# Optimization experiments

Measured on AMD Instinct MI355X. Metric: run time of the kernel, lower is better.

Reference implementation:

```python
import jax, jax.numpy as jnp
import numpy as np

N, E, F_IN, HID, HEADS, NG, NC = 50000, 800000, 128, 64, 4, 64, 10
NEG_SLOPE = 0.2


def gat_conv(h_in, src, dst, W, att_src, att_dst, bias, heads, out_ch, concat, num_nodes):
    # h_in: [N, Fin]; W: [Fin, heads*out_ch]; att_*: [heads, out_ch]; bias: [heads*out_ch] or [out_ch]
    h = (h_in @ W).reshape(num_nodes, heads, out_ch)            # [N,H,C]
    a_src = jnp.sum(h * att_src, axis=-1)                        # [N,H]
    a_dst = jnp.sum(h * att_dst, axis=-1)                        # [N,H]
    alpha = jax.nn.leaky_relu(a_src[src] + a_dst[dst], NEG_SLOPE)  # [Etot,H]
    # softmax over incoming edges per destination node
    amax = jax.ops.segment_max(alpha, dst, num_segments=num_nodes)
    amax = jnp.where(jnp.isfinite(amax), amax, 0.0)
    ex = jnp.exp(alpha - amax[dst])
    denom = jax.ops.segment_sum(ex, dst, num_segments=num_nodes)
    w = ex / (denom[dst] + 1e-16)                                # [Etot,H]
    msg = h[src] * w[:, :, None]                                 # [Etot,H,C]
    out = jax.ops.segment_sum(msg, dst, num_segments=num_nodes)  # [N,H,C]
    out = out.reshape(num_nodes, heads * out_ch) if concat else out.mean(axis=1)
    return out + bias


def setup_inputs() -> dict:
    key = jax.random.key(0)
    ks = jax.random.split(key, 20)
    s = lambda k, shp, f: (jax.random.normal(k, shp, jnp.float32) * f)
    return {
        "x": jax.random.normal(ks[0], (N, F_IN), jnp.float32),
        "edge_index": jax.random.randint(ks[1], (2, E), 0, N, jnp.int32),
        "batch": jax.random.randint(ks[2], (N,), 0, NG, jnp.int32),
        "W_proj": s(ks[3], (F_IN, HID), 0.05), "b_proj": jnp.zeros((HID,), jnp.float32),
        "W1": s(ks[4], (HID, HEADS * HID), 0.05),
        "att_src1": s(ks[5], (HEADS, HID), 0.1), "att_dst1": s(ks[6], (HEADS, HID), 0.1),
        "b1": jnp.zeros((HEADS * HID,), jnp.float32),
        "W2": s(ks[7], (HEADS * HID, HID), 0.05),
        "att_src2": s(ks[8], (1, HID), 0.1), "att_dst2": s(ks[9], (1, HID), 0.1),
        "b2": jnp.zeros((HID,), jnp.float32),
        "W_fc1": s(ks[10], (HID, HID // 2), 0.05), "b_fc1": jnp.zeros((HID // 2,), jnp.float32),
        "W_fc2": s(ks[11], (HID // 2, NC), 0.05), "b_fc2": jnp.zeros((NC,), jnp.float32),
    }


def reference(x, edge_index, batch, W_proj, b_proj, W1, att_src1, att_dst1, b1,
              W2, att_src2, att_dst2, b2, W_fc1, b_fc1, W_fc2, b_fc2):
    n = x.shape[0]
    loops = jnp.arange(n, dtype=edge_index.dtype)  # PyG GATConv add_self_loops=True
    src = jnp.concatenate([edge_index[0], loops])
    dst = jnp.concatenate([edge_index[1], loops])
    h = jax.nn.relu(x @ W_proj + b_proj)                                  # feature_proj + relu
    h = gat_conv(h, src, dst, W1, att_src1, att_dst1, b1, HEADS, HID, True, n)
    h = jax.nn.leaky_relu(h, NEG_SLOPE)                                    # dropout = identity (eval)
    h = gat_conv(h, src, dst, W2, att_src2, att_dst2, b2, 1, HID, False, n)
    h = jax.nn.leaky_relu(h, NEG_SLOPE)
    cnt = jax.ops.segment_sum(jnp.ones((n,), h.dtype), batch, num_segments=NG)
    gmean = jax.ops.segment_sum(h, batch, num_segments=NG) / jnp.maximum(cnt, 1.0)[:, None]
    gmax = jax.ops.segment_max(h, batch, num_segments=NG)
    gmax = jnp.where(jnp.isfinite(gmax), gmax, 0.0)
    g = gmean + gmax
    g = jax.nn.relu(g @ W_fc1 + b_fc1)
    return jax.nn.log_softmax(g @ W_fc2 + b_fc2, axis=1)
```

## Files before the change

### kernel.cpp

```cpp
#include <hip/hip_runtime.h>
#include <math.h>

#define NN 50000
#define EE 800000
#define ET 850000
#define FIN 128
#define HD 64
#define NH 4
#define NGR 64
#define NCL 10
#define NEG 0.2f

typedef unsigned short u16;
typedef unsigned char u8;
typedef unsigned int u32;
typedef __attribute__((ext_vector_type(8))) short short8;
typedef __attribute__((ext_vector_type(4))) float f32x4;

__device__ __forceinline__ float lrelu(float x){ return x > 0.f ? x : NEG * x; }

__device__ __forceinline__ float wsum(float v){
#pragma unroll
  for (int o = 32; o > 0; o >>= 1) v += __shfl_xor(v, o, 64);
  return v;
}
__device__ __forceinline__ float wmax(float v){
#pragma unroll
  for (int o = 32; o > 0; o >>= 1) v = fmaxf(v, __shfl_xor(v, o, 64));
  return v;
}
__device__ __forceinline__ int esrc(const int* ei, int e){ return e < EE ? ei[e] : e - EE; }
__device__ __forceinline__ int edst(const int* ei, int e){ return e < EE ? ei[EE + e] : e - EE; }

__device__ __forceinline__ unsigned f2key(float f){
  unsigned u = __float_as_uint(f);
  return (u & 0x80000000u) ? ~u : (u | 0x80000000u);
}
__device__ __forceinline__ float key2f(unsigned k){
  return (k & 0x80000000u) ? __uint_as_float(k & 0x7fffffffu) : __uint_as_float(~k);
}

__device__ __forceinline__ u16 f2b(float f){
  u32 u = __float_as_uint(f);
  u32 r = (u + 0x7FFFu + ((u >> 16) & 1u)) >> 16;
  return (u16)r;
}
__device__ __forceinline__ float b2f(u16 b){ return __uint_as_float(((u32)b) << 16); }
__device__ __forceinline__ u32 pkbf16(float lo, float hi){
  u32 r;
  asm("v_cvt_pk_bf16_f32 %0, %1, %2" : "=v"(r) : "v"(lo), "v"(hi));
  return r;
}
__device__ __forceinline__ u8 f2fp8(float f){
  return (u8)__builtin_amdgcn_cvt_pk_fp8_f32(f, 0.f, 0, false);
}
__device__ __forceinline__ int rl(int v, int idx){ return __builtin_amdgcn_readlane(v, idx); }
__device__ __forceinline__ float rlf(float v, int idx){
  return __uint_as_float((u32)__builtin_amdgcn_readlane((int)__float_as_uint(v), idx));
}

template<int K, int NOUT, int CPW, bool RELU_BIAS, bool DOTS1, bool DOTS2, bool AF32, bool F8OUT>
__device__ __forceinline__ void gemm_body(int bid, u16* As, float* sred,
            const void* __restrict__ Av, const float* __restrict__ Bf,
            const float* __restrict__ bias, const float* __restrict__ att_s, const float* __restrict__ att_d,
            void* __restrict__ Cv, float* __restrict__ a_s, float* __restrict__ a_d){
  const u16* A = (const u16*)Av;
  const float* Af = (const float*)Av;
  constexpr int KT = K/32;
  constexpr int NT = CPW/16;
  constexpr int LDK = K + 8;
  int t = threadIdx.x, w = t >> 6, l = t & 63;
  int c0 = w*CPW;
  int l16 = l & 15, kg = l >> 4;

  short8 bf[KT*NT];
#pragma unroll
  for (int kt = 0; kt < KT; ++kt)
#pragma unroll
    for (int nt = 0; nt < NT; ++nt){
      int kbase = kt*32 + kg*8;
      int col = c0 + nt*16 + l16;
      short8 v;
#pragma unroll
      for (int j = 0; j < 8; ++j) v[j] = (short)f2b(Bf[(size_t)(kbase + j)*NOUT + col]);
      bf[kt*NT + nt] = v;
    }
  float bv = 0.f;
  if (RELU_BIAS) bv = bias[c0 + l16];
  float asv[NT], adv[NT];
  if (DOTS1 || DOTS2){
#pragma unroll
    for (int nt = 0; nt < NT; ++nt){
      asv[nt] = att_s[c0 + nt*16 + l16];
      adv[nt] = att_d[c0 + nt*16 + l16];
    }
  }

  for (int ch = 0; ch < 2; ++ch){
    int nb = (bid*2 + ch)*64;
    if (nb >= NN) break;
    __syncthreads();
    constexpr int UPR = K/8;
    for (int u = t; u < 64*UPR; u += 256){
      int r = u / UPR, c = u % UPR;
      int n = nb + r;
      uint4 v = make_uint4(0u,0u,0u,0u);
      if (AF32){
        if (n < NN){
          float4 f0 = *(const float4*)&Af[(size_t)n*K + c*8];
          float4 f1 = *(const float4*)&Af[(size_t)n*K + c*8 + 4];
          v = make_uint4(pkbf16(f0.x,f0.y), pkbf16(f0.z,f0.w), pkbf16(f1.x,f1.y), pkbf16(f1.z,f1.w));
        }
      } else {
        if (n < NN) v = *(const uint4*)&A[(size_t)n*K + c*8];
      }
      *(uint4*)&As[r*LDK + c*8] = v;
    }
    __syncthreads();
#pragma unroll
    for (int rt = 0; rt < 4; ++rt){
      short8 af[KT];
#pragma unroll
      for (int kt = 0; kt < KT; ++kt)
        af[kt] = *(const short8*)&As[(rt*16 + l16)*LDK + kt*32 + kg*8];
      f32x4 acc[NT];
#pragma unroll
      for (int nt = 0; nt < NT; ++nt){
        acc[nt] = (f32x4){0.f,0.f,0.f,0.f};
#pragma unroll
        for (int kt = 0; kt < KT; ++kt)
          acc[nt] = __builtin_amdgcn_mfma_f32_16x16x32_bf16(af[kt], bf[kt*NT + nt], acc[nt], 0, 0, 0);
      }
      int rbase = nb + rt*16 + kg*4;
#pragma unroll
      for (int nt = 0; nt < NT; ++nt)
#pragma unroll
        for (int r4 = 0; r4 < 4; ++r4){
          int n = rbase + r4;
          if (n < NN){
            float v = acc[nt][r4];
            if (RELU_BIAS) v = fmaxf(v + bv, 0.f);
            if (F8OUT) ((u8*)Cv)[(size_t)n*NOUT + c0 + nt*16 + l16] = f2fp8(v);
            else       ((u16*)Cv)[(size_t)n*NOUT + c0 + nt*16 + l16] = f2b(v);
          }
        }
      if (DOTS1){
#pragma unroll
        for (int r4 = 0; r4 < 4; ++r4){
          float ps = 0.f, pd = 0.f;
#pragma unroll
          for (int nt = 0; nt < NT; ++nt){
            ps = fmaf(acc[nt][r4], asv[nt], ps);
            pd = fmaf(acc[nt][r4], adv[nt], pd);
          }
#pragma unroll
          for (int o = 1; o < 16; o <<= 1){
            ps += __shfl_xor(ps, o, 64);
            pd += __shfl_xor(pd, o, 64);
          }
          int n = rbase + r4;
          if (l16 == 0 && n < NN){ a_s[n*NH + w] = ps; a_d[n*NH + w] = pd; }
        }
      }
      if (DOTS2){
#pragma unroll
        for (int r4 = 0; r4 < 4; ++r4){
          float ps = acc[0][r4]*asv[0];
          float pd = acc[0][r4]*adv[0];
#pragma unroll
          for (int o = 1; o < 16; o <<= 1){
            ps += __shfl_xor(ps, o, 64);
            pd += __shfl_xor(pd, o, 64);
          }
          if (l16 == 0){
            int row = rt*16 + kg*4 + r4;
            sred[(w*64 + row)*2]     = ps;
            sred[(w*64 + row)*2 + 1] = pd;
          }
        }
      }
    }
    if (DOTS2){
      __syncthreads();
      if (t < 64){
        int n = nb + t;
        if (n < NN){
          float s = sred[t*2] + sred[(64+t)*2] + sred[(128+t)*2] + sred[(192+t)*2];
          float d = sred[t*2+1] + sred[(64+t)*2+1] + sred[(128+t)*2+1] + sred[(192+t)*2+1];
          a_s[n] = s; a_d[n] = d;
        }
      }
    }
  }
}

__global__ __launch_bounds__(256) void k_hist_proj(const int* __restrict__ ei, int* __restrict__ cnt,
            int* __restrict__ rank,
            const float* __restrict__ x, const float* __restrict__ Wp, const float* __restrict__ bp,
            u16* __restrict__ h0b, int gb){
  __shared__ u16 As[64*(FIN+8)];
  int b = blockIdx.x;
  if (b < gb){
    gemm_body<128, 64, 16, true, false, false, true, false>(b, As, nullptr, x, Wp, bp, nullptr, nullptr, h0b, nullptr, nullptr);
  } else {
    int base = (b - gb)*1024;
#pragma unroll
    for (int k = 0; k < 4; ++k){
      int e = base + k*256 + threadIdx.x;
      if (e < ET){
        int d = edst(ei, e);
        rank[e] = atomicAdd(&cnt[d], 1);
      }
    }
  }
}

__global__ void k_bsum(const int* __restrict__ cnt, int* __restrict__ bsums){
  int b = blockIdx.x, t = threadIdx.x;
  int i = b*256 + t;
  int v = (i < NN) ? cnt[i] : 0;
  float s = wsum((float)v);
  __shared__ float ws4[4];
  if ((t & 63) == 0) ws4[t >> 6] = s;
  __syncthreads();
  if (t == 0) bsums[b] = (int)(ws4[0] + ws4[1] + ws4[2] + ws4[3] + 0.5f);
}

__global__ void k_boff(const int* __restrict__ bsums, int* __restrict__ boffs, int nb){
  __shared__ int s[256];
  int t = threadIdx.x;
  int v = (t < nb) ? bsums[t] : 0;
  s[t] = v; __syncthreads();
  for (int d = 1; d < 256; d <<= 1){
    int xv = (t >= d) ? s[t-d] : 0;
    __syncthreads();
    s[t] += xv;
    __syncthreads();
  }
  if (t < nb) boffs[t] = s[t] - v;
}

__global__ void k_off(const int* __restrict__ cnt, const int* __restrict__ boffs,
                      int* __restrict__ off){
  int b = blockIdx.x, t = threadIdx.x;
  int i = b*256 + t;
  __shared__ int s[256];
  int v = (i < NN) ? cnt[i] : 0;
  s[t] = v; __syncthreads();
  for (int d = 1; d < 256; d <<= 1){
    int xv = (t >= d) ? s[t-d] : 0;
    __syncthreads();
    s[t] += xv;
    __syncthreads();
  }
  int excl = s[t] - v;
  if (i < NN) off[i] = boffs[b] + excl;
  if (i == NN - 1) off[NN] = boffs[b] + s[t];
}

__global__ __launch_bounds__(256) void k_scat_feat1(const int* __restrict__ ei, const int* __restrict__ off,
            const int* __restrict__ rank, u16* __restrict__ csrc,
            const u16* __restrict__ h0b, const float* __restrict__ W1,
            const float* __restrict__ as1, const float* __restrict__ ad1,
            u8* __restrict__ h1f8, float* __restrict__ a_s, float* __restrict__ a_d, int gb){
  __shared__ u16 As[64*(HD+8)];
  int b = blockIdx.x;
  if (b < gb){
    gemm_body<64, 256, 64, false, true, false, false, true>(b, As, nullptr, h0b, W1, nullptr, as1, ad1, h1f8, a_s, a_d);
  } else {
    int base = (b - gb)*1024;
#pragma unroll
    for (int k = 0; k < 4; ++k){
      int e = base + k*256 + threadIdx.x;
      if (e < ET){
        int d = edst(ei, e);
        int s = esrc(ei, e);
        csrc[off[d] + rank[e]] = (u16)s;
      }
    }
  }
}

__global__ __launch_bounds__(256) void k_feat2(const u16* __restrict__ h1outb, const float* __restrict__ W2,
            const float* __restrict__ as2, const float* __restrict__ ad2,
            u16* __restrict__ h2b, float* __restrict__ a_s, float* __restrict__ a_d){
  __shared__ u16 As[64*(256+8)];
  __shared__ float sred[4*64*2];
  gemm_body<256, 64, 16, false, false, true, false, false>(blockIdx.x, As, sred, h1outb, W2, nullptr, as2, ad2, h2b, a_s, a_d);
}

__global__ __launch_bounds__(256) void k_gat1(const u8* __restrict__ h1f8, const float* __restrict__ a_s,
                       const float* __restrict__ a_d, const int* __restrict__ off,
                       const u16* __restrict__ csrc, const float* __restrict__ b1,
                       u16* __restrict__ h1outb){
  __shared__ float lw[4][4][68];
  int wv = threadIdx.x >> 6, l = threadIdx.x & 63;
  int n = blockIdx.x*4 + wv;
  if (n >= NN) return;
  int e0 = off[n], e1 = off[n+1], deg = e1 - e0;
  int j16 = l & 15, h = l >> 4;
  float adst = a_d[n*NH + h];
  float acc0 = 0.f, acc1 = 0.f, acc2 = 0.f, acc3 = 0.f;
  const u8* base = h1f8 + 4*l;

#define GAT1_FMA8(wrd, wq) { \
  acc0 = fmaf(__builtin_amdgcn_cvt_f32_fp8((int)(wrd), 0), wq, acc0); \
  acc1 = fmaf(__builtin_amdgcn_cvt_f32_fp8((int)(wrd), 1), wq, acc1); \
  acc2 = fmaf(__builtin_amdgcn_cvt_f32_fp8((int)(wrd), 2), wq, acc2); \
  acc3 = fmaf(__builtin_amdgcn_cvt_f32_fp8((int)(wrd), 3), wq, acc3); }

  if (deg <= 64){
    int sreg[4]; float wreg[4];
#pragma unroll
    for (int c = 0; c < 4; ++c){
      int idx = c*16 + j16;
      int s = (idx < deg) ? (int)csrc[e0 + idx] : 0;
      sreg[c] = s;
      wreg[c] = (idx < deg) ? lrelu(a_s[s*NH + h] + adst) : -3.0e38f;
    }
    float m = fmaxf(fmaxf(wreg[0], wreg[1]), fmaxf(wreg[2], wreg[3]));
#pragma unroll
    for (int o2 = 1; o2 < 16; o2 <<= 1) m = fmaxf(m, __shfl_xor(m, o2, 64));
    float se = 0.f;
#pragma unroll
    for (int c = 0; c < 4; ++c){
      int idx = c*16 + j16;
      float wc = (idx < deg) ? __expf(wreg[c] - m) : 0.f;
      wreg[c] = wc; se += wc;
    }
#pragma unroll
    for (int o2 = 1; o2 < 16; o2 <<= 1) se += __shfl_xor(se, o2, 64);
    float inv = 1.f / (se + 1e-16f);
#pragma unroll
    for (int c = 0; c < 4; ++c) lw[wv][h][c*16 + j16] = wreg[c] * inv;

#pragma unroll
    for (int c = 0; c < 4; ++c){
      int cbase = c*16;
      if (cbase < deg){
        int cnt = deg - cbase; if (cnt > 16) cnt = 16;
        int j2 = 0;
        for (; j2 + 8 <= cnt; j2 += 8){
          float4 wqa = *(const float4*)&lw[wv][h][cbase + j2];
          float4 wqb = *(const float4*)&lw[wv][h][cbase + j2 + 4];
          int s0 = rl(sreg[c], j2),   s1 = rl(sreg[c], j2+1);
          int s2 = rl(sreg[c], j2+2), s3 = rl(sreg[c], j2+3);
          int s4 = rl(sreg[c], j2+4), s5 = rl(sreg[c], j2+5);
          int s6 = rl(sreg[c], j2+6), s7 = rl(sreg[c], j2+7);
          u32 w0 = *(const u32*)(base + (size_t)(u32)s0*256);
          u32 w1 = *(const u32*)(base + (size_t)(u32)s1*256);
          u32 w2 = *(const u32*)(base + (size_t)(u32)s2*256);
          u32 w3 = *(const u32*)(base + (size_t)(u32)s3*256);
          u32 w4 = *(const u32*)(base + (size_t)(u32)s4*256);
          u32 w5 = *(const u32*)(base + (size_t)(u32)s5*256);
          u32 w6 = *(const u32*)(base + (size_t)(u32)s6*256);
          u32 w7 = *(const u32*)(base + (size_t)(u32)s7*256);
          GAT1_FMA8(w0, wqa.x) GAT1_FMA8(w1, wqa.y) GAT1_FMA8(w2, wqa.z) GAT1_FMA8(w3, wqa.w)
          GAT1_FMA8(w4, wqb.x) GAT1_FMA8(w5, wqb.y) GAT1_FMA8(w6, wqb.z) GAT1_FMA8(w7, wqb.w)
        }
        for (; j2 + 4 <= cnt; j2 += 4){
          float4 wq = *(const float4*)&lw[wv][h][cbase + j2];
          int s0 = rl(sreg[c], j2),   s1 = rl(sreg[c], j2+1);
          int s2 = rl(sreg[c], j2+2), s3 = rl(sreg[c], j2+3);
          u32 w0 = *(const u32*)(base + (size_t)(u32)s0*256);
          u32 w1 = *(const u32*)(base + (size_t)(u32)s1*256);
          u32 w2 = *(const u32*)(base + (size_t)(u32)s2*256);
          u32 w3 = *(const u32*)(base + (size_t)(u32)s3*256);
          GAT1_FMA8(w0, wq.x) GAT1_FMA8(w1, wq.y) GAT1_FMA8(w2, wq.z) GAT1_FMA8(w3, wq.w)
        }
        for (; j2 < cnt; ++j2){
          float wqs = lw[wv][h][cbase + j2];
          int s = rl(sreg[c], j2);
          u32 wd = *(const u32*)(base + (size_t)(u32)s*256);
          GAT1_FMA8(wd, wqs)
        }
      }
    }
  } else {
    float m = -3.0e38f;
    for (int i = e0 + j16; i < e1; i += 16){
      int s = csrc[i];
      m = fmaxf(m, lrelu(a_s[s*NH + h] + adst));
    }
#pragma unroll
    for (int o2 = 1; o2 < 16; o2 <<= 1) m = fmaxf(m, __shfl_xor(m, o2, 64));
    float se = 0.f;
    for (int i = e0 + j16; i < e1; i += 16){
      int s = csrc[i];
      se += __expf(lrelu(a_s[s*NH + h] + adst) - m);
    }
#pragma unroll
    for (int o2 = 1; o2 < 16; o2 <<= 1) se += __shfl_xor(se, o2, 64);
    float inv = 1.f / (se + 1e-16f);
    for (int i = e0; i < e1; ++i){
      int s = csrc[i];
      float wq = __expf(lrelu(a_s[s*NH + h] + adst) - m) * inv;
      u32 wd = *(const u32*)(base + (size_t)(u32)s*256);
      GAT1_FMA8(wd, wq)
    }
  }
  float4 bv = *(const float4*)&b1[4*l];
  u32 lo = pkbf16(lrelu(acc0 + bv.x), lrelu(acc1 + bv.y));
  u32 hi = pkbf16(lrelu(acc2 + bv.z), lrelu(acc3 + bv.w));
  *(uint2*)&h1outb[(size_t)n*256 + 4*l] = make_uint2(lo, hi);
}

__global__ __launch_bounds__(256) void k_gat2(const u16* __restrict__ h2b, const float* __restrict__ a_s,
                       const float* __restrict__ a_d, const int* __restrict__ off,
                       const u16* __restrict__ csrc, const float* __restrict__ b2v,
                       float* __restrict__ h2out){
  int wv = threadIdx.x >> 6, l = threadIdx.x & 63;
  int n = blockIdx.x*4 + wv;
  if (n >= NN) return;
  int e0 = off[n], e1 = off[n+1], deg = e1 - e0;
  float adst = a_d[n];
  if (deg <= 64){
    int sA = 0; float alA = -3.0e38f;
    if (l < deg){
      sA = (int)csrc[e0 + l];
      alA = lrelu(a_s[sA] + adst);
    }
    float m = wmax(alA);
    float wA = (l < deg) ? __expf(alA - m) : 0.f;
    float se = wsum(wA);
    wA *= 1.f / (se + 1e-16f);
    float acc = 0.f;
    int idx = 0;
    for (; idx + 8 <= deg; idx += 8){
      int s0 = rl(sA, idx),   s1 = rl(sA, idx+1);
      int s2 = rl(sA, idx+2), s3 = rl(sA, idx+3);
      int s4 = rl(sA, idx+4), s5 = rl(sA, idx+5);
      int s6 = rl(sA, idx+6), s7 = rl(sA, idx+7);
      float w0 = rlf(wA, idx),   w1 = rlf(wA, idx+1);
      float w2 = rlf(wA, idx+2), w3 = rlf(wA, idx+3);
      float w4 = rlf(wA, idx+4), w5 = rlf(wA, idx+5);
      float w6 = rlf(wA, idx+6), w7 = rlf(wA, idx+7);
      float v0 = b2f(h2b[(size_t)(u32)s0*HD + l]);
      float v1 = b2f(h2b[(size_t)(u32)s1*HD + l]);
      float v2 = b2f(h2b[(size_t)(u32)s2*HD + l]);
      float v3 = b2f(h2b[(size_t)(u32)s3*HD + l]);
      float v4 = b2f(h2b[(size_t)(u32)s4*HD + l]);
      float v5 = b2f(h2b[(size_t)(u32)s5*HD + l]);
      float v6 = b2f(h2b[(size_t)(u32)s6*HD + l]);
      float v7 = b2f(h2b[(size_t)(u32)s7*HD + l]);
      acc = fmaf(v0, w0, acc); acc = fmaf(v1, w1, acc);
      acc = fmaf(v2, w2, acc); acc = fmaf(v3, w3, acc);
      acc = fmaf(v4, w4, acc); acc = fmaf(v5, w5, acc);
      acc = fmaf(v6, w6, acc); acc = fmaf(v7, w7, acc);
    }
    for (; idx < deg; ++idx){
      int s = rl(sA, idx);
      float w = rlf(wA, idx);
      acc = fmaf(b2f(h2b[(size_t)(u32)s*HD + l]), w, acc);
    }
    h2out[(size_t)n*HD + l] = lrelu(acc + b2v[l]);
  } else {
    float m = -3.0e38f;
    for (int i = e0 + l; i < e1; i += 64){
      int s = csrc[i];
      m = fmaxf(m, lrelu(a_s[s] + adst));
    }
    m = wmax(m);
    float se = 0.f;
    for (int i = e0 + l; i < e1; i += 64){
      int s = csrc[i];
      se += __expf(lrelu(a_s[s] + adst) - m);
    }
    se = wsum(se);
    float inv = 1.f / (se + 1e-16f);
    float acc = 0.f;
    for (int i = e0; i < e1; ++i){
      int s = csrc[i];
      acc += b2f(h2b[(size_t)s*HD + l]) * __expf(lrelu(a_s[s] + adst) - m);
    }
    h2out[(size_t)n*HD + l] = lrelu(acc*inv + b2v[l]);
  }
}


__global__ void k_pool(const float* __restrict__ h2out, const int* __restrict__ batch,
                       float* __restrict__ gsum, unsigned* __restrict__ gmaxk, int* __restrict__ gcnt){
  __shared__ float ssum[NGR*HD];
  __shared__ unsigned smax[NGR*HD];
  __shared__ int scnt[NGR];
  int t = threadIdx.x;
  for (int i = t; i < NGR*HD; i += 256){ ssum[i] = 0.f; smax[i] = 0u; }
  if (t < NGR) scnt[t] = 0;
  __syncthreads();
  int wv = t >> 6, lane = t & 63;
  for (int n = blockIdx.x*4 + wv; n < NN; n += gridDim.x*4){
    int g = batch[n];
    float v = h2out[(size_t)n*HD + lane];
    atomicAdd(&ssum[g*HD + lane], v);
    atomicMax(&smax[g*HD + lane], f2key(v));
    if (lane == 0) atomicAdd(&scnt[g], 1);
  }
  __syncthreads();
  for (int i = t; i < NGR*HD; i += 256){
    atomicAdd(&gsum[i], ssum[i]);
    atomicMax(&gmaxk[i], smax[i]);
  }
  if (t < NGR) atomicAdd(&gcnt[t], scnt[t]);
}


__global__ void k_final(const float* __restrict__ gsum, const unsigned* __restrict__ gmaxk,
                        const int* __restrict__ gcnt,
                        const float* __restrict__ Wf1, const float* __restrict__ bf1,
                        const float* __restrict__ Wf2, const float* __restrict__ bf2,
                        float* __restrict__ out){
  int g = blockIdx.x, t = threadIdx.x;
  __shared__ float gv[HD];
  __shared__ float f1[32];
  __shared__ float lg[NCL];
  int c = gcnt[g];
  float dn = fmaxf((float)c, 1.f);
  float mean = gsum[g*HD + t] / dn;
  float mx = (c > 0) ? key2f(gmaxk[g*HD + t]) : 0.f;
  gv[t] = mean + mx;
  __syncthreads();
  if (t < 32){
    float a = bf1[t];
#pragma unroll
    for (int k = 0; k < HD; ++k) a += gv[k] * Wf1[k*32 + t];
    f1[t] = a > 0.f ? a : 0.f;
  }
  __syncthreads();
  if (t < NCL){
    float a = bf2[t];
#pragma unroll
    for (int k = 0; k < 32; ++k) a += f1[k] * Wf2[k*NCL + t];
    lg[t] = a;
  }
  __syncthreads();
  if (t < NCL){
    float m = lg[0];
#pragma unroll
    for (int i = 1; i < NCL; ++i) m = fmaxf(m, lg[i]);
    float s = 0.f;
#pragma unroll
    for (int i = 0; i < NCL; ++i) s += expf(lg[i] - m);
    out[g*NCL + t] = lg[t] - m - logf(s);
  }
}

extern "C" void kernel_launch(void* const* d_in, const int* in_sizes, int n_in,
                              void* d_out, int out_size, void* d_ws, size_t ws_size,
                              hipStream_t stream) {
  const float* x   = (const float*)d_in[0];
  const int*   ei  = (const int*)d_in[1];
  const int*   bat = (const int*)d_in[2];
  const float* Wp  = (const float*)d_in[3];
  const float* bp  = (const float*)d_in[4];
  const float* W1  = (const float*)d_in[5];
  const float* as1 = (const float*)d_in[6];
  const float* ad1 = (const float*)d_in[7];
  const float* b1  = (const float*)d_in[8];
  const float* W2  = (const float*)d_in[9];
  const float* as2 = (const float*)d_in[10];
  const float* ad2 = (const float*)d_in[11];
  const float* b2  = (const float*)d_in[12];
  const float* Wf1 = (const float*)d_in[13];
  const float* bf1 = (const float*)d_in[14];
  const float* Wf2 = (const float*)d_in[15];
  const float* bf2 = (const float*)d_in[16];
  float* out = (float*)d_out;

  char* base = (char*)d_ws;
  size_t o = 0;
  auto alloc = [&](size_t elems) -> char* {
    char* p = base + o*4;
    o += (elems + 63) & ~(size_t)63;
    return p;
  };
  u16*   h0b    = (u16*)alloc(1600000);
  u8*    h1f8   = (u8*)alloc(3200000);
  u16*   h1outb = (u16*)alloc(6400000);
  u16*   h2b    = (u16*)alloc(1600000);
  float* h2out  = (float*)alloc(3200000);
  float* a_s1   = (float*)alloc(200000);
  float* a_d1   = (float*)alloc(200000);
  float* a_s2   = (float*)alloc(50000);
  float* a_d2   = (float*)alloc(50000);
  int*   off    = (int*)alloc(50001);
  int*   rank   = (int*)alloc(850000);
  int*   bsums  = (int*)alloc(256);
  int*   boffs  = (int*)alloc(256);
  u16*   csrc   = (u16*)alloc(425000);
  int*   cnt    = (int*)alloc(50000);
  float* gsum   = (float*)alloc(NGR*HD);
  unsigned* gmaxk = (unsigned*)alloc(NGR*HD);
  int*   gcnt   = (int*)alloc(NGR);

  const int NB  = (NN + 255) / 256;
  const int EB4 = (ET + 1023) / 1024;
  const int GB  = (NN + 127) / 128;
  const int WB  = (NN + 3) / 4;

  hipMemsetAsync(cnt, 0, NN*sizeof(int), stream);
  hipMemsetAsync(gsum, 0, (NGR*HD*2 + 64)*sizeof(int), stream);

  k_hist_proj<<<GB + EB4, 256, 0, stream>>>(ei, cnt, rank, x, Wp, bp, h0b, GB);
  k_bsum<<<NB, 256, 0, stream>>>(cnt, bsums);
  k_boff<<<1, 256, 0, stream>>>(bsums, boffs, NB);
  k_off<<<NB, 256, 0, stream>>>(cnt, boffs, off);
  k_scat_feat1<<<GB + EB4, 256, 0, stream>>>(ei, off, rank, csrc, h0b, W1, as1, ad1, h1f8, a_s1, a_d1, GB);

  k_gat1<<<WB, 256, 0, stream>>>(h1f8, a_s1, a_d1, off, csrc, b1, h1outb);

  k_feat2<<<GB, 256, 0, stream>>>(h1outb, W2, as2, ad2, h2b, a_s2, a_d2);
  k_gat2<<<WB, 256, 0, stream>>>(h2b, a_s2, a_d2, off, csrc, b2, h2out);

  k_pool<<<256, 256, 0, stream>>>(h2out, bat, gsum, gmaxk, gcnt);

  k_final<<<NGR, 64, 0, stream>>>(gsum, gmaxk, gcnt, Wf1, bf1, Wf2, bf2, out);
}
```

Measured before the change: 211.7 us.

## Fuse projection and GAT1 feature GEMMs, merge offset scan kernels

Fuses the input projection GEMM with the first GAT linear transform in one kernel, keeping the ReLU'd projected features in shared memory instead of writing them to global and reading them back. The block-offset scan kernel is folded into the offset kernel by having each block reduce the preceding block sums itself, which removes one launch. The edge scatter becomes a standalone kernel. The fused kernel uses more registers and shared memory and puts both GEMMs on the histogram kernel's critical path.

Result: faster. 201.3 us (-4.9%).

```diff
diff --git a/kernel.cpp b/kernel.cpp
--- a/kernel.cpp
+++ b/kernel.cpp
@@ -59,13 +59,135 @@
   return __uint_as_float((u32)__builtin_amdgcn_readlane((int)__float_as_uint(v), idx));
 }
 
-template<int K, int NOUT, int CPW, bool RELU_BIAS, bool DOTS1, bool DOTS2, bool AF32, bool F8OUT>
-__device__ __forceinline__ void gemm_body(int bid, u16* As, float* sred,
-            const void* __restrict__ Av, const float* __restrict__ Bf,
-            const float* __restrict__ bias, const float* __restrict__ att_s, const float* __restrict__ att_d,
-            void* __restrict__ Cv, float* __restrict__ a_s, float* __restrict__ a_d){
-  const u16* A = (const u16*)Av;
-  const float* Af = (const float*)Av;
+__global__ __launch_bounds__(256) void k_phf(const int* __restrict__ ei, int* __restrict__ cnt,
+            int* __restrict__ rank,
+            const float* __restrict__ x, const float* __restrict__ Wp, const float* __restrict__ bp,
+            const float* __restrict__ W1, const float* __restrict__ as1, const float* __restrict__ ad1,
+            u8* __restrict__ h1f8, float* __restrict__ a_s, float* __restrict__ a_d, int gb){
+  __shared__ u16 As[64*(FIN+8)];
+  __shared__ u16 h0s[64*(HD+8)];
+  int b = blockIdx.x;
+  if (b >= gb){
+    int base = (b - gb)*1024;
+#pragma unroll
+    for (int k = 0; k < 4; ++k){
+      int e = base + k*256 + threadIdx.x;
+      if (e < ET){
+        int d = edst(ei, e);
+        rank[e] = atomicAdd(&cnt[d], 1);
+      }
+    }
+    return;
+  }
+  constexpr int LDK1 = FIN + 8;
+  constexpr int LDH  = HD + 8;
+  int t = threadIdx.x, w = t >> 6, l = t & 63;
+  int l16 = l & 15, kg = l >> 4;
+
+  short8 bfp[4];
+#pragma unroll
+  for (int kt = 0; kt < 4; ++kt){
+    short8 v;
+#pragma unroll
+    for (int j = 0; j < 8; ++j) v[j] = (short)f2b(Wp[(size_t)(kt*32 + kg*8 + j)*HD + w*16 + l16]);
+    bfp[kt] = v;
+  }
+  short8 bf1[2*4];
+#pragma unroll
+  for (int kt = 0; kt < 2; ++kt)
+#pragma unroll
+    for (int nt = 0; nt < 4; ++nt){
+      short8 v;
+#pragma unroll
+      for (int j = 0; j < 8; ++j) v[j] = (short)f2b(W1[(size_t)(kt*32 + kg*8 + j)*256 + w*64 + nt*16 + l16]);
+      bf1[kt*4 + nt] = v;
+    }
+  float bv = bp[w*16 + l16];
+  float asv[4], adv[4];
+#pragma unroll
+  for (int nt = 0; nt < 4; ++nt){
+    asv[nt] = as1[w*64 + nt*16 + l16];
+    adv[nt] = ad1[w*64 + nt*16 + l16];
+  }
+
+  for (int ch = 0; ch < 2; ++ch){
+    int nb = (b*2 + ch)*64;
+    if (nb >= NN) break;
+    __syncthreads();
+    for (int u = t; u < 64*16; u += 256){
+      int r = u >> 4, c = u & 15;
+      int n = nb + r;
+      uint4 v = make_uint4(0u,0u,0u,0u);
+      if (n < NN){
+        float4 f0 = *(const float4*)&x[(size_t)n*FIN + c*8];
+        float4 f1 = *(const float4*)&x[(size_t)n*FIN + c*8 + 4];
+        v = make_uint4(pkbf16(f0.x,f0.y), pkbf16(f0.z,f0.w), pkbf16(f1.x,f1.y), pkbf16(f1.z,f1.w));
+      }
+      *(uint4*)&As[r*LDK1 + c*8] = v;
+    }
+    __syncthreads();
+#pragma unroll
+    for (int rt = 0; rt < 4; ++rt){
+      short8 afp[4];
+#pragma unroll
+      for (int kt = 0; kt < 4; ++kt)
+        afp[kt] = *(const short8*)&As[(rt*16 + l16)*LDK1 + kt*32 + kg*8];
+      f32x4 acc = (f32x4){0.f,0.f,0.f,0.f};
+#pragma unroll
+      for (int kt = 0; kt < 4; ++kt)
+        acc = __builtin_amdgcn_mfma_f32_16x16x32_bf16(afp[kt], bfp[kt], acc, 0, 0, 0);
+#pragma unroll
+      for (int r4 = 0; r4 < 4; ++r4)
+        h0s[(rt*16 + kg*4 + r4)*LDH + w*16 + l16] = f2b(fmaxf(acc[r4] + bv, 0.f));
+    }
+    __syncthreads();
+#pragma unroll
+    for (int rt = 0; rt < 4; ++rt){
+      short8 af[2];
+#pragma unroll
+      for (int kt = 0; kt < 2; ++kt)
+        af[kt] = *(const short8*)&h0s[(rt*16 + l16)*LDH + kt*32 + kg*8];
+      f32x4 acc[4];
+#pragma unroll
+      for (int nt = 0; nt < 4; ++nt){
+        acc[nt] = (f32x4){0.f,0.f,0.f,0.f};
+#pragma unroll
+        for (int kt = 0; kt < 2; ++kt)
+          acc[nt] = __builtin_amdgcn_mfma_f32_16x16x32_bf16(af[kt], bf1[kt*4 + nt], acc[nt], 0, 0, 0);
+      }
+      int rbase = nb + rt*16 + kg*4;
+#pragma unroll
+      for (int nt = 0; nt < 4; ++nt)
+#pragma unroll
+        for (int r4 = 0; r4 < 4; ++r4){
+          int n = rbase + r4;
+          if (n < NN) h1f8[(size_t)n*256 + w*64 + nt*16 + l16] = f2fp8(acc[nt][r4]);
+        }
+#pragma unroll
+      for (int r4 = 0; r4 < 4; ++r4){
+        float ps = 0.f, pd = 0.f;
+#pragma unroll
+        for (int nt = 0; nt < 4; ++nt){
+          ps = fmaf(acc[nt][r4], asv[nt], ps);
+          pd = fmaf(acc[nt][r4], adv[nt], pd);
+        }
+#pragma unroll
+        for (int o = 1; o < 16; o <<= 1){
+          ps += __shfl_xor(ps, o, 64);
+          pd += __shfl_xor(pd, o, 64);
+        }
+        int n = rbase + r4;
+        if (l16 == 0 && n < NN){ a_s[n*NH + w] = ps; a_d[n*NH + w] = pd; }
+      }
+    }
+  }
+}
+
+template<int K, int NOUT, int CPW>
+__device__ __forceinline__ void gemm_body2(int bid, u16* As, float* sred,
+            const u16* __restrict__ A, const float* __restrict__ Bf,
+            const float* __restrict__ att_s, const float* __restrict__ att_d,
+            u16* __restrict__ C, float* __restrict__ a_s, float* __restrict__ a_d){
   constexpr int KT = K/32;
   constexpr int NT = CPW/16;
   constexpr int LDK = K + 8;
@@ -85,16 +207,7 @@
       for (int j = 0; j < 8; ++j) v[j] = (short)f2b(Bf[(size_t)(kbase + j)*NOUT + col]);
       bf[kt*NT + nt] = v;
     }
-  float bv = 0.f;
-  if (RELU_BIAS) bv = bias[c0 + l16];
-  float asv[NT], adv[NT];
-  if (DOTS1 || DOTS2){
-#pragma unroll
-    for (int nt = 0; nt < NT; ++nt){
-      asv[nt] = att_s[c0 + nt*16 + l16];
-      adv[nt] = att_d[c0 + nt*16 + l16];
-    }
-  }
+  float asv = att_s[c0 + l16], adv = att_d[c0 + l16];
 
   for (int ch = 0; ch < 2; ++ch){
     int nb = (bid*2 + ch)*64;
@@ -105,15 +218,7 @@
       int r = u / UPR, c = u % UPR;
       int n = nb + r;
       uint4 v = make_uint4(0u,0u,0u,0u);
-      if (AF32){
-        if (n < NN){
-          float4 f0 = *(const float4*)&Af[(size_t)n*K + c*8];
-          float4 f1 = *(const float4*)&Af[(size_t)n*K + c*8 + 4];
-          v = make_uint4(pkbf16(f0.x,f0.y), pkbf16(f0.z,f0.w), pkbf16(f1.x,f1.y), pkbf16(f1.z,f1.w));
-        }
-      } else {
-        if (n < NN) v = *(const uint4*)&A[(size_t)n*K + c*8];
-      }
+      if (n < NN) v = *(const uint4*)&A[(size_t)n*K + c*8];
       *(uint4*)&As[r*LDK + c*8] = v;
     }
     __syncthreads();
@@ -123,93 +228,39 @@
 #pragma unroll
       for (int kt = 0; kt < KT; ++kt)
         af[kt] = *(const short8*)&As[(rt*16 + l16)*LDK + kt*32 + kg*8];
-      f32x4 acc[NT];
-#pragma unroll
-      for (int nt = 0; nt < NT; ++nt){
-        acc[nt] = (f32x4){0.f,0.f,0.f,0.f};
-#pragma unroll
-        for (int kt = 0; kt < KT; ++kt)
-          acc[nt] = __builtin_amdgcn_mfma_f32_16x16x32_bf16(af[kt], bf[kt*NT + nt], acc[nt], 0, 0, 0);
-      }
+      f32x4 acc = (f32x4){0.f,0.f,0.f,0.f};
+#pragma unroll
+      for (int kt = 0; kt < KT; ++kt)
+        acc = __builtin_amdgcn_mfma_f32_16x16x32_bf16(af[kt], bf[kt], acc, 0, 0, 0);
       int rbase = nb + rt*16 + kg*4;
 #pragma unroll
-      for (int nt = 0; nt < NT; ++nt)
-#pragma unroll
-        for (int r4 = 0; r4 < 4; ++r4){
-          int n = rbase + r4;
-          if (n < NN){
-            float v = acc[nt][r4];
-            if (RELU_BIAS) v = fmaxf(v + bv, 0.f);
-            if (F8OUT) ((u8*)Cv)[(size_t)n*NOUT + c0 + nt*16 + l16] = f2fp8(v);
-            else       ((u16*)Cv)[(size_t)n*NOUT + c0 + nt*16 + l16] = f2b(v);
-          }
-        }
-      if (DOTS1){
-#pragma unroll
-        for (int r4 = 0; r4 < 4; ++r4){
-          float ps = 0.f, pd = 0.f;
-#pragma unroll
-          for (int nt = 0; nt < NT; ++nt){
-            ps = fmaf(acc[nt][r4], asv[nt], ps);
-            pd = fmaf(acc[nt][r4], adv[nt], pd);
-          }
-#pragma unroll
-          for (int o = 1; o < 16; o <<= 1){
-            ps += __shfl_xor(ps, o, 64);
-            pd += __shfl_xor(pd, o, 64);
-          }
-          int n = rbase + r4;
-          if (l16 == 0 && n < NN){ a_s[n*NH + w] = ps; a_d[n*NH + w] = pd; }
-        }
-      }
-      if (DOTS2){
-#pragma unroll
-        for (int r4 = 0; r4 < 4; ++r4){
-          float ps = acc[0][r4]*asv[0];
-          float pd = acc[0][r4]*adv[0];
-#pragma unroll
-          for (int o = 1; o < 16; o <<= 1){
-            ps += __shfl_xor(ps, o, 64);
-            pd += __shfl_xor(pd, o, 64);
-          }
-          if (l16 == 0){
-            int row = rt*16 + kg*4 + r4;
-            sred[(w*64 + row)*2]     = ps;
-            sred[(w*64 + row)*2 + 1] = pd;
-          }
-        }
-      }
-    }
-    if (DOTS2){
-      __syncthreads();
-      if (t < 64){
-        int n = nb + t;
-        if (n < NN){
-          float s = sred[t*2] + sred[(64+t)*2] + sred[(128+t)*2] + sred[(192+t)*2];
-          float d = sred[t*2+1] + sred[(64+t)*2+1] + sred[(128+t)*2+1] + sred[(192+t)*2+1];
-          a_s[n] = s; a_d[n] = d;
-        }
-      }
-    }
-  }
-}
-
-__global__ __launch_bounds__(256) void k_hist_proj(const int* __restrict__ ei, int* __restrict__ cnt,
-            int* __restrict__ rank,
-            const float* __restrict__ x, const float* __restrict__ Wp, const float* __restrict__ bp,
-            u16* __restrict__ h0b, int gb){
-  __shared__ u16 As[64*(FIN+8)];
-  int b = blockIdx.x;
-  if (b < gb){
-    gemm_body<128, 64, 16, true, false, false, true, false>(b, As, nullptr, x, Wp, bp, nullptr, nullptr, h0b, nullptr, nullptr);
-  } else {
-    int base = (b - gb)*1024;
-#pragma unroll
-    for (int k = 0; k < 4; ++k){
-      int e = base + k*256 + threadIdx.x;
-      if (e < ET){
-        int d = edst(ei, e);
-        rank[e] = atomicAdd(&cnt[d], 1);
+      for (int r4 = 0; r4 < 4; ++r4){
+        int n = rbase + r4;
+        if (n < NN) C[(size_t)n*NOUT + c0 + l16] = f2b(acc[r4]);
+      }
+#pragma unroll
+      for (int r4 = 0; r4 < 4; ++r4){
+        float ps = acc[r4]*asv;
+        float pd = acc[r4]*adv;
+#pragma unroll
+        for (int o = 1; o < 16; o <<= 1){
+          ps += __shfl_xor(ps, o, 64);
+          pd += __shfl_xor(pd, o, 64);
+        }
+        if (l16 == 0){
+          int row = rt*16 + kg*4 + r4;
+          sred[(w*64 + row)*2]     = ps;
+          sred[(w*64 + row)*2 + 1] = pd;
+        }
+      }
+    }
+    __syncthreads();
+    if (t < 64){
+      int n = nb + t;
+      if (n < NN){
+        float s = sred[t*2] + sred[(64+t)*2] + sred[(128+t)*2] + sred[(192+t)*2];
+        float d = sred[t*2+1] + sred[(64+t)*2+1] + sred[(128+t)*2+1] + sred[(192+t)*2+1];
+        a_s[n] = s; a_d[n] = d;
       }
     }
   }
@@ -226,25 +277,12 @@
   if (t == 0) bsums[b] = (int)(ws4[0] + ws4[1] + ws4[2] + ws4[3] + 0.5f);
 }
 
-__global__ void k_boff(const int* __restrict__ bsums, int* __restrict__ boffs, int nb){
-  __shared__ int s[256];
-  int t = threadIdx.x;
-  int v = (t < nb) ? bsums[t] : 0;
-  s[t] = v; __syncthreads();
-  for (int d = 1; d < 256; d <<= 1){
-    int xv = (t >= d) ? s[t-d] : 0;
-    __syncthreads();
-    s[t] += xv;
-    __syncthreads();
-  }
-  if (t < nb) boffs[t] = s[t] - v;
-}
-
-__global__ void k_off(const int* __restrict__ cnt, const int* __restrict__ boffs,
-                      int* __restrict__ off){
+__global__ __launch_bounds__(256) void k_off2(const int* __restrict__ cnt, const int* __restrict__ bsums,
+                                              int* __restrict__ off){
   int b = blockIdx.x, t = threadIdx.x;
   int i = b*256 + t;
   __shared__ int s[256];
+  __shared__ int w4[4];
   int v = (i < NN) ? cnt[i] : 0;
   s[t] = v; __syncthreads();
   for (int d = 1; d < 256; d <<= 1){
@@ -253,30 +291,27 @@
     s[t] += xv;
     __syncthreads();
   }
-  int excl = s[t] - v;
-  if (i < NN) off[i] = boffs[b] + excl;
-  if (i == NN - 1) off[NN] = boffs[b] + s[t];
-}
-
-__global__ __launch_bounds__(256) void k_scat_feat1(const int* __restrict__ ei, const int* __restrict__ off,
-            const int* __restrict__ rank, u16* __restrict__ csrc,
-            const u16* __restrict__ h0b, const float* __restrict__ W1,
-            const float* __restrict__ as1, const float* __restrict__ ad1,
-            u8* __restrict__ h1f8, float* __restrict__ a_s, float* __restrict__ a_d, int gb){
-  __shared__ u16 As[64*(HD+8)];
-  int b = blockIdx.x;
-  if (b < gb){
-    gemm_body<64, 256, 64, false, true, false, false, true>(b, As, nullptr, h0b, W1, nullptr, as1, ad1, h1f8, a_s, a_d);
-  } else {
-    int base = (b - gb)*1024;
-#pragma unroll
-    for (int k = 0; k < 4; ++k){
-      int e = base + k*256 + threadIdx.x;
-      if (e < ET){
-        int d = edst(ei, e);
-        int s = esrc(ei, e);
-        csrc[off[d] + rank[e]] = (u16)s;
-      }
+  int pv = (t < b) ? bsums[t] : 0;
+  int r = pv;
+#pragma unroll
+  for (int o2 = 32; o2 > 0; o2 >>= 1) r += __shfl_xor(r, o2, 64);
+  if ((t & 63) == 0) w4[t >> 6] = r;
+  __syncthreads();
+  int pre = w4[0] + w4[1] + w4[2] + w4[3];
+  if (i < NN) off[i] = pre + s[t] - v;
+  if (i == NN - 1) off[NN] = pre + s[t];
+}
+
+__global__ __launch_bounds__(256) void k_scatter(const int* __restrict__ ei, const int* __restrict__ off,
+            const int* __restrict__ rank, u16* __restrict__ csrc){
+  int base = blockIdx.x*1024;
+#pragma unroll
+  for (int k = 0; k < 4; ++k){
+    int e = base + k*256 + threadIdx.x;
+    if (e < ET){
+      int d = edst(ei, e);
+      int s = esrc(ei, e);
+      csrc[off[d] + rank[e]] = (u16)s;
     }
   }
 }
@@ -286,7 +321,7 @@
             u16* __restrict__ h2b, float* __restrict__ a_s, float* __restrict__ a_d){
   __shared__ u16 As[64*(256+8)];
   __shared__ float sred[4*64*2];
-  gemm_body<256, 64, 16, false, false, true, false, false>(blockIdx.x, As, sred, h1outb, W2, nullptr, as2, ad2, h2b, a_s, a_d);
+  gemm_body2<256, 64, 16>(blockIdx.x, As, sred, h1outb, W2, as2, ad2, h2b, a_s, a_d);
 }
 
 __global__ __launch_bounds__(256) void k_gat1(const u8* __restrict__ h1f8, const float* __restrict__ a_s,
@@ -573,7 +608,6 @@
     o += (elems + 63) & ~(size_t)63;
     return p;
   };
-  u16*   h0b    = (u16*)alloc(1600000);
   u8*    h1f8   = (u8*)alloc(3200000);
   u16*   h1outb = (u16*)alloc(6400000);
   u16*   h2b    = (u16*)alloc(1600000);
@@ -585,7 +619,6 @@
   int*   off    = (int*)alloc(50001);
   int*   rank   = (int*)alloc(850000);
   int*   bsums  = (int*)alloc(256);
-  int*   boffs  = (int*)alloc(256);
   u16*   csrc   = (u16*)alloc(425000);
   int*   cnt    = (int*)alloc(50000);
   float* gsum   = (float*)alloc(NGR*HD);
@@ -600,11 +633,10 @@
   hipMemsetAsync(cnt, 0, NN*sizeof(int), stream);
   hipMemsetAsync(gsum, 0, (NGR*HD*2 + 64)*sizeof(int), stream);
 
-  k_hist_proj<<<GB + EB4, 256, 0, stream>>>(ei, cnt, rank, x, Wp, bp, h0b, GB);
+  k_phf<<<GB + EB4, 256, 0, stream>>>(ei, cnt, rank, x, Wp, bp, W1, as1, ad1, h1f8, a_s1, a_d1, GB);
   k_bsum<<<NB, 256, 0, stream>>>(cnt, bsums);
-  k_boff<<<1, 256, 0, stream>>>(bsums, boffs, NB);
-  k_off<<<NB, 256, 0, stream>>>(cnt, boffs, off);
-  k_scat_feat1<<<GB + EB4, 256, 0, stream>>>(ei, off, rank, csrc, h0b, W1, as1, ad1, h1f8, a_s1, a_d1, GB);
+  k_off2<<<NB, 256, 0, stream>>>(cnt, bsums, off);
+  k_scatter<<<EB4, 256, 0, stream>>>(ei, off, rank, csrc);
 
   k_gat1<<<WB, 256, 0, stream>>>(h1f8, a_s1, a_d1, off, csrc, b1, h1outb);
 
```
